# Performance work log

Hardware: AMD Instinct MI355X
Metric: run time of the kernel (lower is better)

The kernel has to match this reference:

```python
import jax, jax.numpy as jnp
import numpy as np

B, Z, U, P, X, H = 64, 8, 8, 128, 64, 512
SIGEP_SCALE = 0.1


def _glorot(key, fan_in, fan_out):
    return jax.random.normal(key, (fan_in, fan_out), jnp.float32) * np.sqrt(2.0 / (fan_in + fan_out)).astype(np.float32)


def setup_inputs() -> dict:
    key = jax.random.key(0)
    ks = jax.random.split(key, 8)
    return {
        "x": jax.random.normal(ks[0], (B, X), jnp.float32),
        "Linv": jax.random.normal(ks[1], (B, Z, U, P, P), jnp.float32) * 0.05,
        "Q": jax.random.normal(ks[2], (B, Z, U, 1, P), jnp.float32),
        "W1": _glorot(ks[3], X, H), "b1": jnp.zeros((H,), jnp.float32),
        "W2": _glorot(ks[4], H, H), "b2": jnp.zeros((H,), jnp.float32),
        "W3": _glorot(ks[5], H, H), "b3": jnp.zeros((H,), jnp.float32),
        "W4": _glorot(ks[6], H, P), "b4": jnp.zeros((P,), jnp.float32),
        "logSigEps": jnp.full((U,), np.log(SIGEP_SCALE), jnp.float32),
    }


def reference(x, Linv, Q, W1, b1, W2, b2, W3, b3, W4, b4, logSigEps):
    # encoder: 3 hidden ELU layers + linear head -> phi (B, P)
    h = jax.nn.elu(x @ W1 + b1)
    h = jax.nn.elu(h @ W2 + b2)
    h = jax.nn.elu(h @ W3 + b3)
    phi = h @ W4 + b4  # (B, P)

    Qv = Q[..., 0, :]  # (B, Z, U, P)
    # K = Q @ Linv^T  ->  K[i] = sum_j Q[j] * Linv[i, j]
    K = jnp.einsum('bzuj,bzuij->bzui', Qv, Linv)  # (B, Z, U, P)
    mu = jnp.einsum('bzui,bi->bzu', K, phi)[..., None]  # (B, Z, U, 1)
    # sigma_scale = 1 + phi^T Linv phi
    sigma_scale = 1.0 + jnp.einsum('bi,bzuij,bj->bzu', phi, Linv, phi)  # (B, Z, U)
    pred_cov_diag = jnp.exp(logSigEps) * sigma_scale  # broadcast (U,) over (B, Z, U)
    return mu, pred_cov_diag
```

## Files before the change

kernel.cpp:

```cpp
#include <hip/hip_runtime.h>
#include <math.h>

#define BB 64
#define ZZ 8
#define UU 8
#define PP 128
#define XX 64
#define HH 512

typedef float f32x4 __attribute__((ext_vector_type(4)));

__device__ __forceinline__ float elu(float v) {
    return v > 0.f ? v : (expf(v) - 1.f);
}

template<int K, bool ELU>
__global__ __launch_bounds__(256) void layer_kernel(
    const float* __restrict__ in, const float* __restrict__ W,
    const float* __restrict__ bias, float* __restrict__ out, int N) {
    __shared__ __align__(16) float xs[K];
    __shared__ f32x4 red[8][32];

    const int r   = blockIdx.y;
    const int c0  = blockIdx.x * 128;
    const int tid = threadIdx.x;

    if (tid < K / 4) ((f32x4*)xs)[tid] = ((const f32x4*)(in + (size_t)r * K))[tid];
    __syncthreads();

    const int g    = tid & 31;
    const int ks   = tid >> 5;
    const int kBeg = ks * (K / 8);
    const float* Wp = W + (size_t)kBeg * N + c0 + g * 4;

    f32x4 acc = {0.f, 0.f, 0.f, 0.f};
    #pragma unroll 8
    for (int k = 0; k < K / 8; ++k) {
        const f32x4 w = *(const f32x4*)(Wp + (size_t)k * N);
        const float s = xs[kBeg + k];
        acc.x = fmaf(s, w.x, acc.x);
        acc.y = fmaf(s, w.y, acc.y);
        acc.z = fmaf(s, w.z, acc.z);
        acc.w = fmaf(s, w.w, acc.w);
    }
    red[ks][g] = acc;
    __syncthreads();

    if (tid < 32) {
        f32x4 a = red[0][tid];
        #pragma unroll
        for (int s = 1; s < 8; ++s) {
            const f32x4 b = red[s][tid];
            a.x += b.x; a.y += b.y; a.z += b.z; a.w += b.w;
        }
        const f32x4 bb = *(const f32x4*)(bias + c0 + tid * 4);
        a.x += bb.x; a.y += bb.y; a.z += bb.z; a.w += bb.w;
        if (ELU) { a.x = elu(a.x); a.y = elu(a.y); a.z = elu(a.z); a.w = elu(a.w); }
        *(f32x4*)(out + (size_t)r * N + c0 + tid * 4) = a;
    }
}

__global__ __launch_bounds__(256) void bilinear_kernel(
    const float* __restrict__ Linv, const float* __restrict__ Q,
    const float* __restrict__ phi, const float* __restrict__ logSigEps,
    float* __restrict__ out_mu, float* __restrict__ out_cov) {
    __shared__ __align__(16) float Ps[PP];
    __shared__ __align__(16) float Qs[PP];
    __shared__ float red[8];

    const int bzu = blockIdx.x;
    const int b   = bzu >> 6;
    const int u   = bzu & 7;
    const int tid = threadIdx.x;

    if (tid < 32)      ((f32x4*)Ps)[tid]      = ((const f32x4*)(phi + (size_t)b * PP))[tid];
    else if (tid < 64) ((f32x4*)Qs)[tid - 32] = ((const f32x4*)(Q + (size_t)bzu * PP))[tid - 32];
    __syncthreads();

    const int j0 = (tid & 31) << 2;
    const f32x4 q = *(const f32x4*)(Qs + j0);
    const f32x4 p = *(const f32x4*)(Ps + j0);

    const f32x4* L4 = (const f32x4*)(Linv + (size_t)bzu * (PP * PP));
    float accM = 0.f, accS = 0.f;
    #pragma unroll
    for (int it = 0; it < 16; ++it) {
        const int f = it * 256 + tid;
        const f32x4 L = L4[f];
        const float pi = Ps[f >> 5];
        const float sm = L.x * q.x + L.y * q.y + L.z * q.z + L.w * q.w;
        const float sp = L.x * p.x + L.y * p.y + L.z * p.z + L.w * p.w;
        accM = fmaf(pi, sm, accM);
        accS = fmaf(pi, sp, accS);
    }

    for (int off = 32; off; off >>= 1) {
        accM += __shfl_down(accM, off, 64);
        accS += __shfl_down(accS, off, 64);
    }
    const int wid = tid >> 6;
    if ((tid & 63) == 0) { red[wid] = accM; red[4 + wid] = accS; }
    __syncthreads();
    if (tid == 0) {
        const float m = (red[0] + red[1]) + (red[2] + red[3]);
        const float s = (red[4] + red[5]) + (red[6] + red[7]);
        out_mu[bzu]  = m;
        out_cov[bzu] = expf(logSigEps[u]) * (1.f + s);
    }
}

extern "C" void kernel_launch(void* const* d_in, const int* in_sizes, int n_in,
                              void* d_out, int out_size, void* d_ws, size_t ws_size,
                              hipStream_t stream) {
    const float* x         = (const float*)d_in[0];
    const float* Linv      = (const float*)d_in[1];
    const float* Q         = (const float*)d_in[2];
    const float* W1        = (const float*)d_in[3];
    const float* b1        = (const float*)d_in[4];
    const float* W2        = (const float*)d_in[5];
    const float* b2        = (const float*)d_in[6];
    const float* W3        = (const float*)d_in[7];
    const float* b3        = (const float*)d_in[8];
    const float* W4        = (const float*)d_in[9];
    const float* b4        = (const float*)d_in[10];
    const float* logSigEps = (const float*)d_in[11];

    float* ws  = (float*)d_ws;
    float* h1  = ws;
    float* h2  = ws + BB * HH;
    float* phi = ws + 2 * BB * HH;

    layer_kernel<XX, true ><<<dim3(4, BB), 256, 0, stream>>>(x,  W1, b1, h1,  HH);
    layer_kernel<HH, true ><<<dim3(4, BB), 256, 0, stream>>>(h1, W2, b2, h2,  HH);
    layer_kernel<HH, true ><<<dim3(4, BB), 256, 0, stream>>>(h2, W3, b3, h1,  HH);
    layer_kernel<HH, false><<<dim3(1, BB), 256, 0, stream>>>(h1, W4, b4, phi, PP);

    float* out_mu  = (float*)d_out;
    float* out_cov = out_mu + BB * ZZ * UU;

    bilinear_kernel<<<BB * ZZ * UU, 256, 0, stream>>>(Linv, Q, phi, logSigEps,
                                                      out_mu, out_cov);
}
```

Baseline: 69.19 us.

## Fuse MLP layers into one cooperative kernel with grid syncs

```diff
diff --git a/kernel.cpp b/kernel.cpp
--- a/kernel.cpp
+++ b/kernel.cpp
@@ -1,5 +1,8 @@
 #include <hip/hip_runtime.h>
+#include <hip/hip_cooperative_groups.h>
 #include <math.h>
+
+namespace cg = cooperative_groups;
 
 #define BB 64
 #define ZZ 8
@@ -9,55 +12,101 @@
 #define HH 512
 
 typedef float f32x4 __attribute__((ext_vector_type(4)));
+typedef float f32x2 __attribute__((ext_vector_type(2)));
 
 __device__ __forceinline__ float elu(float v) {
     return v > 0.f ? v : (expf(v) - 1.f);
 }
 
-template<int K, bool ELU>
-__global__ __launch_bounds__(256) void layer_kernel(
-    const float* __restrict__ in, const float* __restrict__ W,
-    const float* __restrict__ bias, float* __restrict__ out, int N) {
-    __shared__ __align__(16) float xs[K];
-    __shared__ f32x4 red[8][32];
-
-    const int r   = blockIdx.y;
-    const int c0  = blockIdx.x * 128;
-    const int tid = threadIdx.x;
-
-    if (tid < K / 4) ((f32x4*)xs)[tid] = ((const f32x4*)(in + (size_t)r * K))[tid];
-    __syncthreads();
-
-    const int g    = tid & 31;
-    const int ks   = tid >> 5;
-    const int kBeg = ks * (K / 8);
+template<int K, int NCOLS, bool ELU>
+__device__ __forceinline__ void chunk_gemv(
+    const float* __restrict__ hs, const float* __restrict__ W,
+    const float* __restrict__ bias, float* __restrict__ outRow,
+    int N, int c0, int tid, f32x4* __restrict__ red) {
+    constexpr int GROUPS = NCOLS / 4;
+    constexpr int SLICES = 256 / GROUPS;
+    constexpr int KPER   = K / SLICES;
+    const int g    = tid % GROUPS;
+    const int ks   = tid / GROUPS;
+    const int kBeg = ks * KPER;
     const float* Wp = W + (size_t)kBeg * N + c0 + g * 4;
 
     f32x4 acc = {0.f, 0.f, 0.f, 0.f};
     #pragma unroll 8
-    for (int k = 0; k < K / 8; ++k) {
+    for (int k = 0; k < KPER; ++k) {
         const f32x4 w = *(const f32x4*)(Wp + (size_t)k * N);
-        const float s = xs[kBeg + k];
+        const float s = hs[kBeg + k];
         acc.x = fmaf(s, w.x, acc.x);
         acc.y = fmaf(s, w.y, acc.y);
         acc.z = fmaf(s, w.z, acc.z);
         acc.w = fmaf(s, w.w, acc.w);
     }
-    red[ks][g] = acc;
+    red[ks * (GROUPS + 1) + g] = acc;
     __syncthreads();
 
-    if (tid < 32) {
-        f32x4 a = red[0][tid];
+    if (tid < GROUPS) {
+        f32x4 a = red[tid];
         #pragma unroll
-        for (int s = 1; s < 8; ++s) {
-            const f32x4 b = red[s][tid];
+        for (int s2 = 1; s2 < SLICES; ++s2) {
+            const f32x4 b = red[s2 * (GROUPS + 1) + tid];
             a.x += b.x; a.y += b.y; a.z += b.z; a.w += b.w;
         }
         const f32x4 bb = *(const f32x4*)(bias + c0 + tid * 4);
         a.x += bb.x; a.y += bb.y; a.z += bb.z; a.w += bb.w;
         if (ELU) { a.x = elu(a.x); a.y = elu(a.y); a.z = elu(a.z); a.w = elu(a.w); }
-        *(f32x4*)(out + (size_t)r * N + c0 + tid * 4) = a;
+        *(f32x4*)(outRow + c0 + tid * 4) = a;
     }
+    __syncthreads();
+}
+
+__global__ __launch_bounds__(256) void mlp_coop(
+    const float* __restrict__ x,
+    const float* __restrict__ W1, const float* __restrict__ b1,
+    const float* __restrict__ W2, const float* __restrict__ b2,
+    const float* __restrict__ W3, const float* __restrict__ b3,
+    const float* __restrict__ W4, const float* __restrict__ b4,
+    float* __restrict__ h2buf, float* __restrict__ h3buf,
+    float* __restrict__ phi) {
+    cg::grid_group grid = cg::this_grid();
+
+    __shared__ __align__(16) float xs[XX];
+    __shared__ __align__(16) float hs[HH];
+    __shared__ __align__(16) f32x4 red[288];
+
+    const int tid = threadIdx.x;
+    const int r   = blockIdx.x >> 2;
+    const int c   = blockIdx.x & 3;
+
+    if (tid < XX) xs[tid] = x[(size_t)r * XX + tid];
+    __syncthreads();
+    {
+        const f32x2* W = (const f32x2*)W1;
+        f32x2 a0 = {0.f, 0.f}, a1 = {0.f, 0.f};
+        #pragma unroll 8
+        for (int k = 0; k < XX; k += 2) {
+            const f32x2 w0 = W[(k + 0) * (HH / 2) + tid];
+            const f32x2 w1 = W[(k + 1) * (HH / 2) + tid];
+            const float s0 = xs[k + 0], s1 = xs[k + 1];
+            a0.x = fmaf(s0, w0.x, a0.x); a0.y = fmaf(s0, w0.y, a0.y);
+            a1.x = fmaf(s1, w1.x, a1.x); a1.y = fmaf(s1, w1.y, a1.y);
+        }
+        const f32x2 bb = ((const f32x2*)b1)[tid];
+        hs[2 * tid + 0] = elu(a0.x + a1.x + bb.x);
+        hs[2 * tid + 1] = elu(a0.y + a1.y + bb.y);
+    }
+    __syncthreads();
+
+    chunk_gemv<HH, 128, true>(hs, W2, b2, h2buf + (size_t)r * HH, HH, c * 128, tid, red);
+    grid.sync();
+
+    ((f32x2*)hs)[tid] = ((const f32x2*)(h2buf + (size_t)r * HH))[tid];
+    __syncthreads();
+    chunk_gemv<HH, 128, true>(hs, W3, b3, h3buf + (size_t)r * HH, HH, c * 128, tid, red);
+    grid.sync();
+
+    ((f32x2*)hs)[tid] = ((const f32x2*)(h3buf + (size_t)r * HH))[tid];
+    __syncthreads();
+    chunk_gemv<HH, 32, false>(hs, W4, b4, phi + (size_t)r * PP, PP, c * 32, tid, red);
 }
 
 __global__ __launch_bounds__(256) void bilinear_kernel(
@@ -126,14 +175,15 @@
     const float* logSigEps = (const float*)d_in[11];
 
     float* ws  = (float*)d_ws;
-    float* h1  = ws;
-    float* h2  = ws + BB * HH;
+    float* h2  = ws;
+    float* h3  = ws + BB * HH;
     float* phi = ws + 2 * BB * HH;
 
-    layer_kernel<XX, true ><<<dim3(4, BB), 256, 0, stream>>>(x,  W1, b1, h1,  HH);
-    layer_kernel<HH, true ><<<dim3(4, BB), 256, 0, stream>>>(h1, W2, b2, h2,  HH);
-    layer_kernel<HH, true ><<<dim3(4, BB), 256, 0, stream>>>(h2, W3, b3, h1,  HH);
-    layer_kernel<HH, false><<<dim3(1, BB), 256, 0, stream>>>(h1, W4, b4, phi, PP);
+    void* args[] = {(void*)&x, (void*)&W1, (void*)&b1, (void*)&W2, (void*)&b2,
+                    (void*)&W3, (void*)&b3, (void*)&W4, (void*)&b4,
+                    (void*)&h2, (void*)&h3, (void*)&phi};
+    hipLaunchCooperativeKernel(reinterpret_cast<void*>(mlp_coop),
+                               dim3(BB * 4), dim3(256), args, 0, stream);
 
     float* out_mu  = (float*)d_out;
     float* out_cov = out_mu + BB * ZZ * UU;
```

Result: slower. 122.8 us (+77.5%).
